# Kernel optimization log

Hardware: AMD Instinct MI355X
Metric: run time of the kernel (lower is better)

The kernel has to match this reference:

```python
import jax, jax.numpy as jnp
import numpy as np

N_PE = 100000   # num 'pe' nodes
N_R = 100000    # num 'router' nodes
E = 600000      # edges per relation
D_IN = 64       # input feature dim per node type
H = 128         # hidden_channels
G = 64          # graphs in batch


def setup_inputs() -> dict:
    key = jax.random.key(0)
    ks = jax.random.split(key, 20)
    inp = {}
    inp["x_pe"] = jax.random.normal(ks[0], (N_PE, D_IN), jnp.float32)
    inp["x_r"] = jax.random.normal(ks[1], (N_R, D_IN), jnp.float32)
    # edge_index per relation: row0 = src node ids, row1 = dst node ids
    inp["ei_per"] = jax.random.randint(ks[2], (2, E), 0, N_PE, jnp.int32)   # pe -> router
    inp["ei_rpe"] = jax.random.randint(ks[3], (2, E), 0, N_R, jnp.int32)    # router -> pe
    inp["ei_rr"] = jax.random.randint(ks[4], (2, E), 0, N_R, jnp.int32)     # router -> router
    inp["batch_pe"] = jnp.sort(jax.random.randint(ks[5], (N_PE,), 0, G, jnp.int32))
    inp["batch_r"] = jnp.sort(jax.random.randint(ks[6], (N_R,), 0, G, jnp.int32))
    # GraphConv params, relation axis ordered [pe->router, router->pe, router->router]
    s1 = 1.0 / np.sqrt(D_IN)
    s2 = 1.0 / np.sqrt(H)
    inp["Wrel1"] = jax.random.normal(ks[7], (3, D_IN, H), jnp.float32) * s1
    inp["brel1"] = jnp.zeros((3, H), jnp.float32)
    inp["Wroot1"] = jax.random.normal(ks[8], (3, D_IN, H), jnp.float32) * s1
    inp["Wrel23"] = jax.random.normal(ks[9], (2, 3, H, H), jnp.float32) * s2
    inp["brel23"] = jnp.zeros((2, 3, H), jnp.float32)
    inp["Wroot23"] = jax.random.normal(ks[10], (2, 3, H, H), jnp.float32) * s2
    # per-node-type MLP heads, type axis ordered [pe, router]
    inp["mlp_W1"] = jax.random.normal(ks[11], (2, H, 5), jnp.float32) * s2
    inp["mlp_b1"] = jnp.zeros((2, 5), jnp.float32)
    inp["mlp_W2"] = jax.random.normal(ks[12], (2, 5, 1), jnp.float32) * (1.0 / np.sqrt(5.0))
    inp["mlp_b2"] = jnp.zeros((2, 1), jnp.float32)
    inp["out_W"] = jax.random.normal(ks[13], (2, 1), jnp.float32) * (1.0 / np.sqrt(2.0))
    inp["out_b"] = jnp.zeros((1,), jnp.float32)
    return inp


def _hetero_graphconv(x_pe, x_r, ei_per, ei_rpe, ei_rr, Wrel, brel, Wroot):
    # GraphConv: lin_rel(scatter_add(x_src)) + lin_root(x_dst); to_hetero sums per dst type.
    agg_r_from_pe = jax.ops.segment_sum(x_pe[ei_per[0]], ei_per[1], num_segments=N_R)
    agg_pe_from_r = jax.ops.segment_sum(x_r[ei_rpe[0]], ei_rpe[1], num_segments=N_PE)
    agg_r_from_r = jax.ops.segment_sum(x_r[ei_rr[0]], ei_rr[1], num_segments=N_R)
    o_pe = agg_pe_from_r @ Wrel[1] + brel[1] + x_pe @ Wroot[1]
    o_r = (agg_r_from_pe @ Wrel[0] + brel[0] + x_r @ Wroot[0]) \
        + (agg_r_from_r @ Wrel[2] + brel[2] + x_r @ Wroot[2])
    return o_pe, o_r


def reference(x_pe, x_r, ei_per, ei_rpe, ei_rr, batch_pe, batch_r,
              Wrel1, brel1, Wroot1, Wrel23, brel23, Wroot23,
              mlp_W1, mlp_b1, mlp_W2, mlp_b2, out_W, out_b):
    h_pe, h_r = _hetero_graphconv(x_pe, x_r, ei_per, ei_rpe, ei_rr, Wrel1, brel1, Wroot1)
    h_pe, h_r = jax.nn.relu(h_pe), jax.nn.relu(h_r)
    h_pe, h_r = _hetero_graphconv(h_pe, h_r, ei_per, ei_rpe, ei_rr, Wrel23[0], brel23[0], Wroot23[0])
    h_pe, h_r = jax.nn.relu(h_pe), jax.nn.relu(h_r)
    h_pe, h_r = _hetero_graphconv(h_pe, h_r, ei_per, ei_rpe, ei_rr, Wrel23[1], brel23[1], Wroot23[1])
    gm_pe = jax.ops.segment_max(h_pe, batch_pe, num_segments=G)  # [G, H]
    gm_r = jax.ops.segment_max(h_r, batch_r, num_segments=G)
    def mlp(x, W1, b1, W2, b2):
        return jax.nn.relu(x @ W1 + b1) @ W2 + b2
    o_pe = mlp(gm_pe, mlp_W1[0], mlp_b1[0], mlp_W2[0], mlp_b2[0])  # [G, 1]
    o_r = mlp(gm_r, mlp_W1[1], mlp_b1[1], mlp_W2[1], mlp_b2[1])
    cat = jnp.concatenate([o_pe, o_r], axis=1)  # [G, 2]
    return cat @ out_W + out_b  # [G, 1]
```

## Files before the change

### kernel.cpp

```cpp
#include <hip/hip_runtime.h>
#include <cstddef>
#include <cstdint>

#define DIN 64
#define HID 128
#define NBKMAX 256
#define EPB 2048

typedef _Float16 half4v __attribute__((ext_vector_type(4)));
typedef _Float16 half8v __attribute__((ext_vector_type(8)));
typedef float f32x16 __attribute__((ext_vector_type(16)));

__device__ __forceinline__ unsigned encf(float f) {
    unsigned b = __float_as_uint(f);
    return (b & 0x80000000u) ? ~b : (b | 0x80000000u);
}
__device__ __forceinline__ float decf(unsigned u) {
    unsigned b = (u & 0x80000000u) ? (u & 0x7FFFFFFFu) : ~u;
    return __uint_as_float(b);
}

__global__ void matadd3_k(const float* a0, const float* b0f, float* o0, int n0,
                          const float* a1, const float* b1f, float* o1, int n1,
                          const float* a2, const float* b2f, float* o2, int n2) {
    int r = blockIdx.y;
    const float* a = r == 0 ? a0 : (r == 1 ? a1 : a2);
    const float* b = r == 0 ? b0f : (r == 1 ? b1f : b2f);
    float* o = r == 0 ? o0 : (r == 1 ? o1 : o2);
    int n = r == 0 ? n0 : (r == 1 ? n1 : n2);
    int i = blockIdx.x * 256 + threadIdx.x;
    if (i < n) o[i] = a[i] + b[i];
}

__global__ void conv_x2_k(const float* s0, _Float16* d0, int n40,
                          const float* s1, _Float16* d1, int n41) {
    int r = blockIdx.y;
    const float* s = r == 0 ? s0 : s1;
    _Float16* d = r == 0 ? d0 : d1;
    int n4 = r == 0 ? n40 : n41;
    int i = blockIdx.x * 256 + threadIdx.x;
    if (i >= n4) return;
    float4 v = *reinterpret_cast<const float4*>(&s[i * 4]);
    half4v h;
    h.x = (_Float16)v.x; h.y = (_Float16)v.y; h.z = (_Float16)v.z; h.w = (_Float16)v.w;
    *reinterpret_cast<half4v*>(&d[i * 4]) = h;
}

struct CW { const float* src; _Float16* dst; int K; int total; };
__global__ void conv_w7_k(CW c0, CW c1, CW c2, CW c3, CW c4, CW c5, CW c6) {
    CW J;
    switch (blockIdx.y) {
        case 0: J = c0; break; case 1: J = c1; break; case 2: J = c2; break;
        case 3: J = c3; break; case 4: J = c4; break; case 5: J = c5; break;
        default: J = c6; break;
    }
    int i = blockIdx.x * 256 + threadIdx.x;
    if (i >= J.total) return;
    int m = i / (J.K * HID);
    int rem = i % (J.K * HID);
    int k = rem / HID;
    int col = rem % HID;
    J.dst[(size_t)m * HID * J.K + (size_t)col * J.K + k] = (_Float16)J.src[i];
}

__global__ __launch_bounds__(256) void bhist_k(const int* e0, const int* e1, const int* e2, int E,
                                               int* c0, int* c1, int* c2) {
    int r = blockIdx.y;
    const int* ei = r == 0 ? e0 : (r == 1 ? e1 : e2);
    int* cnt = r == 0 ? c0 : (r == 1 ? c1 : c2);
    __shared__ int sc[NBKMAX];
    int t = threadIdx.x;
    sc[t] = 0;
    __syncthreads();
    int base = blockIdx.x * EPB;
    int n = min(EPB, E - base);
    for (int i = t; i < n; i += 256)
        atomicAdd(&sc[(unsigned)ei[E + base + i] >> 9], 1);
    __syncthreads();
    if (sc[t]) atomicAdd(&cnt[t], sc[t]);
}

__global__ __launch_bounds__(256) void bscan_k(int* c0, int* bb0, int* cu0, int* rp0, int n0,
                                               int* c1, int* bb1, int* cu1, int* rp1, int n1,
                                               int* c2, int* bb2, int* cu2, int* rp2, int n2,
                                               int E) {
    __shared__ int sh[256];
    int t = threadIdx.x;
    for (int r = 0; r < 3; ++r) {
        int* cnt = r == 0 ? c0 : (r == 1 ? c1 : c2);
        int* bb  = r == 0 ? bb0 : (r == 1 ? bb1 : bb2);
        int* cu  = r == 0 ? cu0 : (r == 1 ? cu1 : cu2);
        int* rp  = r == 0 ? rp0 : (r == 1 ? rp1 : rp2);
        int N    = r == 0 ? n0 : (r == 1 ? n1 : n2);
        int v = cnt[t];
        sh[t] = v;
        __syncthreads();
        for (int off = 1; off < 256; off <<= 1) {
            int val = (t >= off) ? sh[t - off] : 0;
            __syncthreads();
            sh[t] += val;
            __syncthreads();
        }
        int ex = sh[t] - v;
        bb[t] = ex;
        cu[t] = ex;
        if (t == 255) bb[256] = sh[255];
        if (t == 0) rp[N] = E;
        __syncthreads();
    }
}

__global__ __launch_bounds__(256) void bin_k(const int* e0, const int* e1, const int* e2, int E,
                                             int* cu0, int* cu1, int* cu2,
                                             unsigned* t0, unsigned* t1, unsigned* t2) {
    int r = blockIdx.y;
    const int* ei = r == 0 ? e0 : (r == 1 ? e1 : e2);
    int* gcur = r == 0 ? cu0 : (r == 1 ? cu1 : cu2);
    unsigned* temp = r == 0 ? t0 : (r == 1 ? t1 : t2);
    __shared__ unsigned pk[EPB];
    __shared__ unsigned short bkb[EPB];
    __shared__ int cnt[NBKMAX];
    __shared__ int scn[NBKMAX];
    __shared__ int rb[NBKMAX];
    int t = threadIdx.x;
    int base = blockIdx.x * EPB;
    int n = min(EPB, E - base);
    cnt[t] = 0;
    __syncthreads();
    for (int i = t; i < n; i += 256)
        atomicAdd(&cnt[(unsigned)ei[E + base + i] >> 9], 1);
    __syncthreads();
    {
        int v = cnt[t];
        scn[t] = v;
        __syncthreads();
        for (int off = 1; off < 256; off <<= 1) {
            int val = (t >= off) ? scn[t - off] : 0;
            __syncthreads();
            scn[t] += val;
            __syncthreads();
        }
        int ex = scn[t] - v;
        __syncthreads();
        scn[t] = ex;
    }
    {
        int c = cnt[t];
        rb[t] = c ? atomicAdd(&gcur[t], c) : 0;
        cnt[t] = 0;
    }
    __syncthreads();
    for (int i = t; i < n; i += 256) {
        int s = ei[base + i];
        int d = ei[E + base + i];
        int b = (unsigned)d >> 9;
        int slot = scn[b] + atomicAdd(&cnt[b], 1);
        pk[slot] = ((unsigned)s << 9) | (unsigned)(d & 511);
        bkb[slot] = (unsigned short)b;
    }
    __syncthreads();
    for (int i = t; i < n; i += 256) {
        int b = bkb[i];
        temp[rb[b] + (i - scn[b])] = pk[i];
    }
}

__global__ __launch_bounds__(256) void bcsr_k(const unsigned* t0, const unsigned* t1, const unsigned* t2,
                                              const int* bb0, const int* bb1, const int* bb2,
                                              int* rp0, int* rp1, int* rp2,
                                              int* a0, int* a1, int* a2,
                                              int n0, int n1, int n2) {
    int r = blockIdx.y;
    const unsigned* temp = r == 0 ? t0 : (r == 1 ? t1 : t2);
    const int* bb = r == 0 ? bb0 : (r == 1 ? bb1 : bb2);
    int* rp = r == 0 ? rp0 : (r == 1 ? rp1 : rp2);
    int* adj = r == 0 ? a0 : (r == 1 ? a1 : a2);
    int N = r == 0 ? n0 : (r == 1 ? n1 : n2);
    int b = blockIdx.x;
    int lo = bb[b], hi = bb[b + 1];
    __shared__ int cnt[512];
    __shared__ int sh[256];
    int t = threadIdx.x;
    cnt[t] = 0; cnt[t + 256] = 0;
    __syncthreads();
    for (int i = lo + t; i < hi; i += 256)
        atomicAdd(&cnt[temp[i] & 511], 1);
    __syncthreads();
    int c0 = cnt[2 * t], c1 = cnt[2 * t + 1];
    sh[t] = c0 + c1;
    __syncthreads();
    for (int off = 1; off < 256; off <<= 1) {
        int v = (t >= off) ? sh[t - off] : 0;
        __syncthreads();
        sh[t] += v;
        __syncthreads();
    }
    int pairExcl = sh[t] - (c0 + c1);
    __syncthreads();
    int e0x = lo + pairExcl;
    int e1x = e0x + c0;
    cnt[2 * t] = e0x;
    cnt[2 * t + 1] = e1x;
    int nodeBase = b * 512;
    if (nodeBase + 2 * t < N) rp[nodeBase + 2 * t] = e0x;
    if (nodeBase + 2 * t + 1 < N) rp[nodeBase + 2 * t + 1] = e1x;
    __syncthreads();
    for (int i = lo + t; i < hi; i += 256) {
        unsigned p = temp[i];
        int pos = atomicAdd(&cnt[p & 511], 1);
        adj[pos] = p >> 9;
    }
}

struct AJob { const _Float16* X; const int* rp; const int* adj; _Float16* AGG; int N; int gb; };
template <int D>
__global__ __launch_bounds__(256) void gather3_k(AJob a0, AJob a1, AJob a2) {
    int b = blockIdx.x;
    AJob J;
    if (b < a0.gb) { J = a0; }
    else if (b < a0.gb + a1.gb) { J = a1; b -= a0.gb; }
    else { J = a2; b -= a0.gb + a1.gb; }
    constexpr int TPN = D / 8;
    constexpr int NPB = 256 / TPN;
    int node = b * NPB + threadIdx.x / TPN;
    int lane = threadIdx.x % TPN;
    if (node >= J.N) return;
    int a = J.rp[node], e1 = J.rp[node + 1];
    float acc[8] = {0.f, 0.f, 0.f, 0.f, 0.f, 0.f, 0.f, 0.f};
    int e = a;
    for (; e + 4 <= e1; e += 4) {
        int s0 = J.adj[e], s1 = J.adj[e + 1], s2 = J.adj[e + 2], s3 = J.adj[e + 3];
        half8v v0 = *reinterpret_cast<const half8v*>(&J.X[(size_t)s0 * D + lane * 8]);
        half8v v1 = *reinterpret_cast<const half8v*>(&J.X[(size_t)s1 * D + lane * 8]);
        half8v v2 = *reinterpret_cast<const half8v*>(&J.X[(size_t)s2 * D + lane * 8]);
        half8v v3 = *reinterpret_cast<const half8v*>(&J.X[(size_t)s3 * D + lane * 8]);
#pragma unroll
        for (int i = 0; i < 8; ++i) acc[i] += (float)v0[i] + (float)v1[i] + (float)v2[i] + (float)v3[i];
    }
    for (; e < e1; ++e) {
        int s0 = J.adj[e];
        half8v v0 = *reinterpret_cast<const half8v*>(&J.X[(size_t)s0 * D + lane * 8]);
#pragma unroll
        for (int i = 0; i < 8; ++i) acc[i] += (float)v0[i];
    }
    half8v o;
#pragma unroll
    for (int i = 0; i < 8; ++i) o[i] = (_Float16)acc[i];
    *reinterpret_cast<half8v*>(&J.AGG[(size_t)node * D + lane * 8]) = o;
}

struct GJob {
    const _Float16* A0; const _Float16* A1; const _Float16* A2;
    const _Float16* W0; const _Float16* W1; const _Float16* W2;
    const float* b0; const float* b1;
    _Float16* O;
    int N; int total; int gb;
};

template <bool RELU>
__global__ __launch_bounds__(256) void gemm2_k(GJob j0, GJob j1, int K, int lg) {
    const bool second = ((int)blockIdx.x >= j0.gb);
    const GJob J = second ? j1 : j0;
    const int bx = blockIdx.x - (second ? j0.gb : 0);
    __shared__ _Float16 Alds[2][128 * 64];
    const int tid = threadIdx.x;
    const int lane = tid & 63;
    const int w = tid >> 6;
    const int wr = w & 1, wc = w >> 1;
    const int rowBase = bx * 128;

    f32x16 acc[2][2];
#pragma unroll
    for (int r = 0; r < 2; ++r)
#pragma unroll
        for (int c = 0; c < 2; ++c)
#pragma unroll
            for (int q = 0; q < 16; ++q) acc[r][c][q] = 0.0f;

    const _Float16* Ap[3] = {J.A0, J.A1, J.A2};

    const int row = tid & 127;
    const int kh = (tid >> 7) * 32;
    const int gr = rowBase + row;
    const bool rowOK = (gr < J.N);
    int offW[4];
#pragma unroll
    for (int j = 0; j < 4; ++j) {
        int t = (kh >> 4) + (j >> 1);
        int k8 = j & 1;
        offW[j] = (((row >> 5) * 4 + t) * 64 + (row & 31) + 32 * k8) * 8;
    }

    const int total = J.total;
    const int cmask = (1 << lg) - 1;

    auto ld = [&](int c, half8v h[4]) {
        int s = c >> lg;
        int k0 = (c & cmask) * 64;
        half8v z = {};
        h[0] = z; h[1] = z; h[2] = z; h[3] = z;
        if (rowOK) {
            const _Float16* p = Ap[s] + (size_t)gr * K + k0 + kh;
#pragma unroll
            for (int j = 0; j < 4; ++j) h[j] = *reinterpret_cast<const half8v*>(p + j * 8);
        }
    };

    half8v cur[4], nxt[4];
    ld(0, cur);
#pragma unroll
    for (int j = 0; j < 4; ++j) *reinterpret_cast<half8v*>(&Alds[0][offW[j]]) = cur[j];
    __syncthreads();

    for (int c = 0; c < total; ++c) {
        if (c + 1 < total) ld(c + 1, nxt);
        int s = c >> lg;
        int wk0 = (c & cmask) * 64;
        const _Float16* __restrict__ Wt = (s == 0) ? J.W0 : (s == 1 ? J.W1 : J.W2);
        const _Float16* buf = Alds[c & 1];
#pragma unroll
        for (int t = 0; t < 4; ++t) {
            half8v av[2], wv[2];
#pragma unroll
            for (int r = 0; r < 2; ++r) {
                int R = (wr * 2 + r) * 4 + t;
                av[r] = *reinterpret_cast<const half8v*>(&buf[(R * 64 + lane) * 8]);
            }
#pragma unroll
            for (int cc = 0; cc < 2; ++cc) {
                int col = wc * 64 + cc * 32 + (lane & 31);
                wv[cc] = *reinterpret_cast<const half8v*>(
                    &Wt[(size_t)col * K + wk0 + t * 16 + (lane >> 5) * 8]);
            }
#pragma unroll
            for (int r = 0; r < 2; ++r)
#pragma unroll
                for (int cc = 0; cc < 2; ++cc)
                    acc[r][cc] = __builtin_amdgcn_mfma_f32_32x32x16_f16(wv[cc], av[r], acc[r][cc], 0, 0, 0);
        }
        if (c + 1 < total) {
            _Float16* nb = Alds[(c + 1) & 1];
#pragma unroll
            for (int j = 0; j < 4; ++j) *reinterpret_cast<half8v*>(&nb[offW[j]]) = nxt[j];
        }
        __syncthreads();
    }

#pragma unroll
    for (int r = 0; r < 2; ++r) {
        int node = rowBase + (wr * 2 + r) * 32 + (lane & 31);
        if (node >= J.N) continue;
        _Float16* orow = J.O + (size_t)node * HID;
#pragma unroll
        for (int cc = 0; cc < 2; ++cc) {
            int fb_ = wc * 64 + cc * 32 + 4 * (lane >> 5);
#pragma unroll
            for (int g = 0; g < 4; ++g) {
                int f = fb_ + g * 8;
                float4 bv = *reinterpret_cast<const float4*>(&J.b0[f]);
                if (J.b1) {
                    float4 b2v = *reinterpret_cast<const float4*>(&J.b1[f]);
                    bv.x += b2v.x; bv.y += b2v.y; bv.z += b2v.z; bv.w += b2v.w;
                }
                half4v hv;
#pragma unroll
                for (int i = 0; i < 4; ++i) {
                    float v = acc[r][cc][g * 4 + i] + ((const float*)&bv)[i];
                    if (RELU) v = fmaxf(v, 0.f);
                    hv[i] = (_Float16)v;
                }
                *reinterpret_cast<half4v*>(&orow[f]) = hv;
            }
        }
    }
}

__global__ void seg_bounds2_k(const int* b0, int n0, int* s0,
                              const int* b1, int n1, int* s1, int G) {
    int r = blockIdx.x;
    const int* batch = r == 0 ? b0 : b1;
    int n = r == 0 ? n0 : n1;
    int* starts = r == 0 ? s0 : s1;
    int g = threadIdx.x;
    if (g > G) return;
    int lo = 0, hi = n;
    while (lo < hi) {
        int mid = (lo + hi) >> 1;
        if (batch[mid] < g) lo = mid + 1; else hi = mid;
    }
    starts[g] = lo;
}

__global__ __launch_bounds__(128) void seg_max2_k(const _Float16* H0, const int* st0, unsigned* g0,
                                                  const _Float16* H1, const int* st1, unsigned* g1) {
    int z = blockIdx.z;
    const _Float16* Hf = z == 0 ? H0 : H1;
    const int* starts = z == 0 ? st0 : st1;
    unsigned* gmU = z == 0 ? g0 : g1;
    int g = blockIdx.x;
    int sub = blockIdx.y;
    int SUB = gridDim.y;
    int f = threadIdx.x;
    int s0 = starts[g], s1 = starts[g + 1];
    int len = s1 - s0;
    if (len <= 0) return;
    int chunk = (len + SUB - 1) / SUB;
    int a = s0 + sub * chunk;
    int b = min(a + chunk, s1);
    if (a >= b) return;
    float m = -__builtin_huge_valf();
    for (int n = a; n < b; ++n) m = fmaxf(m, (float)Hf[(size_t)n * HID + f]);
    atomicMax(&gmU[g * HID + f], encf(m));
}

__global__ void head_k(const unsigned* __restrict__ gmU_pe, const unsigned* __restrict__ gmU_r,
                       const float* __restrict__ W1, const float* __restrict__ b1,
                       const float* __restrict__ W2, const float* __restrict__ b2,
                       const float* __restrict__ oW, const float* __restrict__ ob,
                       float* __restrict__ out, int G) {
    int g = threadIdx.x;
    if (g >= G) return;
    float vals[2];
#pragma unroll
    for (int t = 0; t < 2; ++t) {
        const unsigned* gm = t ? gmU_r : gmU_pe;
        float z[5];
#pragma unroll
        for (int j = 0; j < 5; ++j) z[j] = b1[t * 5 + j];
        for (int f = 0; f < HID; ++f) {
            float x = decf(gm[g * HID + f]);
#pragma unroll
            for (int j = 0; j < 5; ++j) z[j] = fmaf(x, W1[t * HID * 5 + f * 5 + j], z[j]);
        }
        float o = b2[t];
#pragma unroll
        for (int j = 0; j < 5; ++j) o = fmaf(fmaxf(z[j], 0.f), W2[t * 5 + j], o);
        vals[t] = o;
    }
    out[g] = vals[0] * oW[0] + vals[1] * oW[1] + ob[0];
}

extern "C" void kernel_launch(void* const* d_in, const int* in_sizes, int n_in,
                              void* d_out, int out_size, void* d_ws, size_t ws_size,
                              hipStream_t stream) {
    const float* x_pe    = (const float*)d_in[0];
    const float* x_r     = (const float*)d_in[1];
    const int* ei_per    = (const int*)d_in[2];
    const int* ei_rpe    = (const int*)d_in[3];
    const int* ei_rr     = (const int*)d_in[4];
    const int* batch_pe  = (const int*)d_in[5];
    const int* batch_r   = (const int*)d_in[6];
    const float* Wrel1   = (const float*)d_in[7];
    const float* brel1   = (const float*)d_in[8];
    const float* Wroot1  = (const float*)d_in[9];
    const float* Wrel23  = (const float*)d_in[10];
    const float* brel23  = (const float*)d_in[11];
    const float* Wroot23 = (const float*)d_in[12];
    const float* mlp_W1  = (const float*)d_in[13];
    const float* mlp_b1  = (const float*)d_in[14];
    const float* mlp_W2  = (const float*)d_in[15];
    const float* mlp_b2  = (const float*)d_in[16];
    const float* out_W   = (const float*)d_in[17];
    const float* out_b   = (const float*)d_in[18];
    float* out = (float*)d_out;

    const int N_PE = in_sizes[0] / DIN;
    const int N_R  = in_sizes[1] / DIN;
    const int E    = in_sizes[2] / 2;
    const int G    = out_size;
    const int NMAX = (N_PE > N_R) ? N_PE : N_R;
    const size_t SZM = (size_t)NMAX * HID;

    _Float16* H1 = (_Float16*)d_ws;
    _Float16* H2 = H1 + SZM;
    _Float16* H3 = H2 + SZM;
    _Float16* H4 = H3 + SZM;
    _Float16* H5 = H4 + SZM;
    _Float16* xh_pe = H5 + SZM;
    _Float16* xh_r  = xh_pe + (size_t)N_PE * DIN;
    float* wsum1 = (float*)(xh_r + (size_t)N_R * DIN);
    float* wsum2 = wsum1 + DIN * HID;
    float* wsum3 = wsum2 + HID * HID;
    _Float16* wt_rel1    = (_Float16*)(wsum3 + HID * HID);
    _Float16* wt_root1pe = wt_rel1 + 3 * DIN * HID;
    _Float16* wt_wsum1   = wt_root1pe + DIN * HID;
    _Float16* wt_rel23   = wt_wsum1 + DIN * HID;
    _Float16* wt_root23  = wt_rel23 + 6 * HID * HID;
    _Float16* wt_wsum2   = wt_root23 + 6 * HID * HID;
    _Float16* wt_wsum3   = wt_wsum2 + HID * HID;
    unsigned* gmU_pe = (unsigned*)(wt_wsum3 + HID * HID);
    unsigned* gmU_r  = gmU_pe + G * HID;
    int* starts_pe = (int*)(gmU_r + G * HID);
    int* starts_r  = starts_pe + (G + 1);
    int* bktCnt = starts_r + (G + 1);
    int* bb     = bktCnt + 3 * NBKMAX;
    int* gcur   = bb + 3 * (NBKMAX + 1);
    int* csr    = gcur + 3 * NBKMAX;
    const size_t relstride = (size_t)(NMAX + 1) + 2 * (size_t)E + 16;

    int* rp[3]; int* adjp[3]; unsigned* tmp[3];
    const int Nds[3] = {N_R, N_PE, N_R};
    for (int r = 0; r < 3; ++r) {
        int* rowptr = csr + (size_t)r * relstride;
        rp[r] = rowptr;
        adjp[r] = rowptr + (Nds[r] + 1);
        tmp[r] = (unsigned*)(adjp[r] + E);
    }

    const int gpe = (N_PE + 127) / 128, grr = (N_R + 127) / 128;

    {
        dim3 g((16384 + 255) / 256, 3);
        matadd3_k<<<g, 256, 0, stream>>>(
            Wroot1, Wroot1 + 2 * DIN * HID, wsum1, DIN * HID,
            Wroot23, Wroot23 + 2 * HID * HID, wsum2, HID * HID,
            Wroot23 + 3 * HID * HID, Wroot23 + 5 * HID * HID, wsum3, HID * HID);
    }
    {
        int n40 = N_PE * DIN / 4, n41 = N_R * DIN / 4;
        int nmax = n40 > n41 ? n40 : n41;
        dim3 g((nmax + 255) / 256, 2);
        conv_x2_k<<<g, 256, 0, stream>>>(x_pe, xh_pe, n40, x_r, xh_r, n41);
    }
    {
        CW c0{Wrel1, wt_rel1, DIN, 3 * DIN * HID};
        CW c1{Wroot1 + 1 * DIN * HID, wt_root1pe, DIN, DIN * HID};
        CW c2{wsum1, wt_wsum1, DIN, DIN * HID};
        CW c3{Wrel23, wt_rel23, HID, 6 * HID * HID};
        CW c4{Wroot23, wt_root23, HID, 6 * HID * HID};
        CW c5{wsum2, wt_wsum2, HID, HID * HID};
        CW c6{wsum3, wt_wsum3, HID, HID * HID};
        dim3 g((6 * HID * HID + 255) / 256, 7);
        conv_w7_k<<<g, 256, 0, stream>>>(c0, c1, c2, c3, c4, c5, c6);
    }
    {
        hipMemsetAsync(bktCnt, 0, 3 * NBKMAX * sizeof(int), stream);
        int eb = (E + EPB - 1) / EPB;
        dim3 gh(eb, 3);
        bhist_k<<<gh, 256, 0, stream>>>(ei_per, ei_rpe, ei_rr, E,
                                        bktCnt, bktCnt + NBKMAX, bktCnt + 2 * NBKMAX);
        bscan_k<<<1, 256, 0, stream>>>(
            bktCnt, bb, gcur, rp[0], Nds[0],
            bktCnt + NBKMAX, bb + (NBKMAX + 1), gcur + NBKMAX, rp[1], Nds[1],
            bktCnt + 2 * NBKMAX, bb + 2 * (NBKMAX + 1), gcur + 2 * NBKMAX, rp[2], Nds[2], E);
        bin_k<<<gh, 256, 0, stream>>>(ei_per, ei_rpe, ei_rr, E,
                                      gcur, gcur + NBKMAX, gcur + 2 * NBKMAX,
                                      tmp[0], tmp[1], tmp[2]);
        dim3 gc(NBKMAX, 3);
        bcsr_k<<<gc, 256, 0, stream>>>(tmp[0], tmp[1], tmp[2],
                                       bb, bb + (NBKMAX + 1), bb + 2 * (NBKMAX + 1),
                                       rp[0], rp[1], rp[2],
                                       adjp[0], adjp[1], adjp[2],
                                       Nds[0], Nds[1], Nds[2]);
    }

    {
        AJob a0{xh_r, rp[1], adjp[1], H1, N_PE, (N_PE + 31) / 32};
        AJob a1{xh_pe, rp[0], adjp[0], H2, N_R, (N_R + 31) / 32};
        AJob a2{xh_r, rp[2], adjp[2], H3, N_R, (N_R + 31) / 32};
        gather3_k<DIN><<<a0.gb + a1.gb + a2.gb, 256, 0, stream>>>(a0, a1, a2);
        GJob jp{H1, xh_pe, nullptr,
                wt_rel1 + 1 * DIN * HID, wt_root1pe, nullptr,
                brel1 + HID, nullptr, H4, N_PE, 2, gpe};
        GJob jr{H2, H3, xh_r,
                wt_rel1, wt_rel1 + 2 * DIN * HID, wt_wsum1,
                brel1, brel1 + 2 * HID, H5, N_R, 3, grr};
        gemm2_k<true><<<gpe + grr, 256, 0, stream>>>(jp, jr, DIN, 0);
    }
    {
        AJob a0{H5, rp[1], adjp[1], H1, N_PE, (N_PE + 15) / 16};
        AJob a1{H4, rp[0], adjp[0], H2, N_R, (N_R + 15) / 16};
        AJob a2{H5, rp[2], adjp[2], H3, N_R, (N_R + 15) / 16};
        gather3_k<HID><<<a0.gb + a1.gb + a2.gb, 256, 0, stream>>>(a0, a1, a2);
        GJob jp{H1, H4, nullptr,
                wt_rel23 + 1 * HID * HID, wt_root23 + 1 * HID * HID, nullptr,
                brel23 + HID, nullptr, H1, N_PE, 2 * 2, gpe};
        GJob jr{H2, H3, H5,
                wt_rel23, wt_rel23 + 2 * HID * HID, wt_wsum2,
                brel23, brel23 + 2 * HID, H2, N_R, 3 * 2, grr};
        gemm2_k<true><<<gpe + grr, 256, 0, stream>>>(jp, jr, HID, 1);
    }
    {
        AJob a0{H2, rp[1], adjp[1], H3, N_PE, (N_PE + 15) / 16};
        AJob a1{H1, rp[0], adjp[0], H4, N_R, (N_R + 15) / 16};
        AJob a2{H2, rp[2], adjp[2], H5, N_R, (N_R + 15) / 16};
        gather3_k<HID><<<a0.gb + a1.gb + a2.gb, 256, 0, stream>>>(a0, a1, a2);
        GJob jp{H3, H1, nullptr,
                wt_rel23 + 4 * HID * HID, wt_root23 + 4 * HID * HID, nullptr,
                brel23 + 4 * HID, nullptr, H3, N_PE, 2 * 2, gpe};
        GJob jr{H4, H5, H2,
                wt_rel23 + 3 * HID * HID, wt_rel23 + 5 * HID * HID, wt_wsum3,
                brel23 + 3 * HID, brel23 + 5 * HID, H4, N_R, 3 * 2, grr};
        gemm2_k<false><<<gpe + grr, 256, 0, stream>>>(jp, jr, HID, 1);
    }

    seg_bounds2_k<<<2, 128, 0, stream>>>(batch_pe, N_PE, starts_pe, batch_r, N_R, starts_r, G);
    hipMemsetAsync(gmU_pe, 0, 2 * (size_t)G * HID * sizeof(unsigned), stream);
    dim3 gs(G, 16, 2);
    seg_max2_k<<<gs, 128, 0, stream>>>(H3, starts_pe, gmU_pe, H4, starts_r, gmU_r);
    head_k<<<1, 64, 0, stream>>>(gmU_pe, gmU_r, mlp_W1, mlp_b1, mlp_W2, mlp_b2, out_W, out_b, out, G);
}
```

Baseline: 629.4 us.

## Stage weight tiles in LDS for GEMM and fuse root-weight sums into conversion

The GEMM kernel now loads each 128x64 weight chunk into shared memory alongside the A tile, instead of having every wave read weight fragments straight from global memory. The A tile goes from double-buffered to single-buffered, with an extra barrier per chunk. Separately, the matadd kernel that summed root weights is folded into the weight conversion kernel through an optional second source, removing one launch and only converting the root weights actually used. The extra barrier and lost double buffering may expose load latency.

```diff
diff --git a/kernel.cpp b/kernel.cpp
--- a/kernel.cpp
+++ b/kernel.cpp
@@ -18,18 +18,6 @@
 __device__ __forceinline__ float decf(unsigned u) {
     unsigned b = (u & 0x80000000u) ? (u & 0x7FFFFFFFu) : ~u;
     return __uint_as_float(b);
-}
-
-__global__ void matadd3_k(const float* a0, const float* b0f, float* o0, int n0,
-                          const float* a1, const float* b1f, float* o1, int n1,
-                          const float* a2, const float* b2f, float* o2, int n2) {
-    int r = blockIdx.y;
-    const float* a = r == 0 ? a0 : (r == 1 ? a1 : a2);
-    const float* b = r == 0 ? b0f : (r == 1 ? b1f : b2f);
-    float* o = r == 0 ? o0 : (r == 1 ? o1 : o2);
-    int n = r == 0 ? n0 : (r == 1 ? n1 : n2);
-    int i = blockIdx.x * 256 + threadIdx.x;
-    if (i < n) o[i] = a[i] + b[i];
 }
 
 __global__ void conv_x2_k(const float* s0, _Float16* d0, int n40,
@@ -46,13 +34,13 @@
     *reinterpret_cast<half4v*>(&d[i * 4]) = h;
 }
 
-struct CW { const float* src; _Float16* dst; int K; int total; };
-__global__ void conv_w7_k(CW c0, CW c1, CW c2, CW c3, CW c4, CW c5, CW c6) {
+struct CW { const float* src; const float* src2; _Float16* dst; int K; int total; };
+__global__ void conv_w8_k(CW c0, CW c1, CW c2, CW c3, CW c4, CW c5, CW c6, CW c7) {
     CW J;
     switch (blockIdx.y) {
         case 0: J = c0; break; case 1: J = c1; break; case 2: J = c2; break;
         case 3: J = c3; break; case 4: J = c4; break; case 5: J = c5; break;
-        default: J = c6; break;
+        case 6: J = c6; break; default: J = c7; break;
     }
     int i = blockIdx.x * 256 + threadIdx.x;
     if (i >= J.total) return;
@@ -60,7 +48,9 @@
     int rem = i % (J.K * HID);
     int k = rem / HID;
     int col = rem % HID;
-    J.dst[(size_t)m * HID * J.K + (size_t)col * J.K + k] = (_Float16)J.src[i];
+    float v = J.src[i];
+    if (J.src2) v += J.src2[i];
+    J.dst[(size_t)m * HID * J.K + (size_t)col * J.K + k] = (_Float16)v;
 }
 
 __global__ __launch_bounds__(256) void bhist_k(const int* e0, const int* e1, const int* e2, int E,
@@ -262,7 +252,8 @@
     const bool second = ((int)blockIdx.x >= j0.gb);
     const GJob J = second ? j1 : j0;
     const int bx = blockIdx.x - (second ? j0.gb : 0);
-    __shared__ _Float16 Alds[2][128 * 64];
+    __shared__ _Float16 Alds[128 * 64];
+    __shared__ _Float16 Wlds[128 * 64];
     const int tid = threadIdx.x;
     const int lane = tid & 63;
     const int w = tid >> 6;
@@ -283,18 +274,18 @@
     const int kh = (tid >> 7) * 32;
     const int gr = rowBase + row;
     const bool rowOK = (gr < J.N);
-    int offW[4];
+    int offS[4];
 #pragma unroll
     for (int j = 0; j < 4; ++j) {
         int t = (kh >> 4) + (j >> 1);
         int k8 = j & 1;
-        offW[j] = (((row >> 5) * 4 + t) * 64 + (row & 31) + 32 * k8) * 8;
+        offS[j] = (((row >> 5) * 4 + t) * 64 + (row & 31) + 32 * k8) * 8;
     }
 
     const int total = J.total;
     const int cmask = (1 << lg) - 1;
 
-    auto ld = [&](int c, half8v h[4]) {
+    auto ldA = [&](int c, half8v h[4]) {
         int s = c >> lg;
         int k0 = (c & cmask) * 64;
         half8v z = {};
@@ -305,45 +296,51 @@
             for (int j = 0; j < 4; ++j) h[j] = *reinterpret_cast<const half8v*>(p + j * 8);
         }
     };
-
-    half8v cur[4], nxt[4];
-    ld(0, cur);
-#pragma unroll
-    for (int j = 0; j < 4; ++j) *reinterpret_cast<half8v*>(&Alds[0][offW[j]]) = cur[j];
+    auto ldW = [&](int c, half8v h[4]) {
+        int s = c >> lg;
+        int k0 = (c & cmask) * 64;
+        const _Float16* __restrict__ Wt = (s == 0) ? J.W0 : (s == 1 ? J.W1 : J.W2);
+        const _Float16* p = Wt + (size_t)row * K + k0 + kh;
+#pragma unroll
+        for (int j = 0; j < 4; ++j) h[j] = *reinterpret_cast<const half8v*>(p + j * 8);
+    };
+
+    half8v ra[4], rw[4];
+    ldA(0, ra); ldW(0, rw);
+#pragma unroll
+    for (int j = 0; j < 4; ++j) {
+        *reinterpret_cast<half8v*>(&Alds[offS[j]]) = ra[j];
+        *reinterpret_cast<half8v*>(&Wlds[offS[j]]) = rw[j];
+    }
     __syncthreads();
 
     for (int c = 0; c < total; ++c) {
-        if (c + 1 < total) ld(c + 1, nxt);
-        int s = c >> lg;
-        int wk0 = (c & cmask) * 64;
-        const _Float16* __restrict__ Wt = (s == 0) ? J.W0 : (s == 1 ? J.W1 : J.W2);
-        const _Float16* buf = Alds[c & 1];
+        const bool more = (c + 1 < total);
+        if (more) { ldA(c + 1, ra); ldW(c + 1, rw); }
 #pragma unroll
         for (int t = 0; t < 4; ++t) {
             half8v av[2], wv[2];
 #pragma unroll
-            for (int r = 0; r < 2; ++r) {
-                int R = (wr * 2 + r) * 4 + t;
-                av[r] = *reinterpret_cast<const half8v*>(&buf[(R * 64 + lane) * 8]);
-            }
-#pragma unroll
-            for (int cc = 0; cc < 2; ++cc) {
-                int col = wc * 64 + cc * 32 + (lane & 31);
-                wv[cc] = *reinterpret_cast<const half8v*>(
-                    &Wt[(size_t)col * K + wk0 + t * 16 + (lane >> 5) * 8]);
-            }
+            for (int r = 0; r < 2; ++r)
+                av[r] = *reinterpret_cast<const half8v*>(&Alds[(((wr * 2 + r) * 4 + t) * 64 + lane) * 8]);
+#pragma unroll
+            for (int cc = 0; cc < 2; ++cc)
+                wv[cc] = *reinterpret_cast<const half8v*>(&Wlds[(((wc * 2 + cc) * 4 + t) * 64 + lane) * 8]);
 #pragma unroll
             for (int r = 0; r < 2; ++r)
 #pragma unroll
                 for (int cc = 0; cc < 2; ++cc)
                     acc[r][cc] = __builtin_amdgcn_mfma_f32_32x32x16_f16(wv[cc], av[r], acc[r][cc], 0, 0, 0);
         }
-        if (c + 1 < total) {
-            _Float16* nb = Alds[(c + 1) & 1];
-#pragma unroll
-            for (int j = 0; j < 4; ++j) *reinterpret_cast<half8v*>(&nb[offW[j]]) = nxt[j];
-        }
-        __syncthreads();
+        __syncthreads();
+        if (more) {
+#pragma unroll
+            for (int j = 0; j < 4; ++j) {
+                *reinterpret_cast<half8v*>(&Alds[offS[j]]) = ra[j];
+                *reinterpret_cast<half8v*>(&Wlds[offS[j]]) = rw[j];
+            }
+            __syncthreads();
+        }
     }
 
 #pragma unroll
@@ -478,15 +475,13 @@
     _Float16* H5 = H4 + SZM;
     _Float16* xh_pe = H5 + SZM;
     _Float16* xh_r  = xh_pe + (size_t)N_PE * DIN;
-    float* wsum1 = (float*)(xh_r + (size_t)N_R * DIN);
-    float* wsum2 = wsum1 + DIN * HID;
-    float* wsum3 = wsum2 + HID * HID;
-    _Float16* wt_rel1    = (_Float16*)(wsum3 + HID * HID);
+    _Float16* wt_rel1    = xh_r + (size_t)N_R * DIN;
     _Float16* wt_root1pe = wt_rel1 + 3 * DIN * HID;
     _Float16* wt_wsum1   = wt_root1pe + DIN * HID;
     _Float16* wt_rel23   = wt_wsum1 + DIN * HID;
-    _Float16* wt_root23  = wt_rel23 + 6 * HID * HID;
-    _Float16* wt_wsum2   = wt_root23 + 6 * HID * HID;
+    _Float16* wt_root_l2 = wt_rel23 + 6 * HID * HID;
+    _Float16* wt_root_l3 = wt_root_l2 + HID * HID;
+    _Float16* wt_wsum2   = wt_root_l3 + HID * HID;
     _Float16* wt_wsum3   = wt_wsum2 + HID * HID;
     unsigned* gmU_pe = (unsigned*)(wt_wsum3 + HID * HID);
     unsigned* gmU_r  = gmU_pe + G * HID;
@@ -510,28 +505,22 @@
     const int gpe = (N_PE + 127) / 128, grr = (N_R + 127) / 128;
 
     {
-        dim3 g((16384 + 255) / 256, 3);
-        matadd3_k<<<g, 256, 0, stream>>>(
-            Wroot1, Wroot1 + 2 * DIN * HID, wsum1, DIN * HID,
-            Wroot23, Wroot23 + 2 * HID * HID, wsum2, HID * HID,
-            Wroot23 + 3 * HID * HID, Wroot23 + 5 * HID * HID, wsum3, HID * HID);
-    }
-    {
         int n40 = N_PE * DIN / 4, n41 = N_R * DIN / 4;
         int nmax = n40 > n41 ? n40 : n41;
         dim3 g((nmax + 255) / 256, 2);
         conv_x2_k<<<g, 256, 0, stream>>>(x_pe, xh_pe, n40, x_r, xh_r, n41);
     }
     {
-        CW c0{Wrel1, wt_rel1, DIN, 3 * DIN * HID};
-        CW c1{Wroot1 + 1 * DIN * HID, wt_root1pe, DIN, DIN * HID};
-        CW c2{wsum1, wt_wsum1, DIN, DIN * HID};
-        CW c3{Wrel23, wt_rel23, HID, 6 * HID * HID};
-        CW c4{Wroot23, wt_root23, HID, 6 * HID * HID};
-        CW c5{wsum2, wt_wsum2, HID, HID * HID};
-        CW c6{wsum3, wt_wsum3, HID, HID * HID};
-        dim3 g((6 * HID * HID + 255) / 256, 7);
-        conv_w7_k<<<g, 256, 0, stream>>>(c0, c1, c2, c3, c4, c5, c6);
+        CW c0{Wrel1, nullptr, wt_rel1, DIN, 3 * DIN * HID};
+        CW c1{Wroot1 + 1 * DIN * HID, nullptr, wt_root1pe, DIN, DIN * HID};
+        CW c2{Wroot1, Wroot1 + 2 * DIN * HID, wt_wsum1, DIN, DIN * HID};
+        CW c3{Wrel23, nullptr, wt_rel23, HID, 6 * HID * HID};
+        CW c4{Wroot23 + 1 * HID * HID, nullptr, wt_root_l2, HID, HID * HID};
+        CW c5{Wroot23 + 4 * HID * HID, nullptr, wt_root_l3, HID, HID * HID};
+        CW c6{Wroot23, Wroot23 + 2 * HID * HID, wt_wsum2, HID, HID * HID};
+        CW c7{Wroot23 + 3 * HID * HID, Wroot23 + 5 * HID * HID, wt_wsum3, HID, HID * HID};
+        dim3 g((6 * HID * HID + 255) / 256, 8);
+        conv_w8_k<<<g, 256, 0, stream>>>(c0, c1, c2, c3, c4, c5, c6, c7);
     }
     {
         hipMemsetAsync(bktCnt, 0, 3 * NBKMAX * sizeof(int), stream);
@@ -573,7 +562,7 @@
         AJob a2{H5, rp[2], adjp[2], H3, N_R, (N_R + 15) / 16};
         gather3_k<HID><<<a0.gb + a1.gb + a2.gb, 256, 0, stream>>>(a0, a1, a2);
         GJob jp{H1, H4, nullptr,
-                wt_rel23 + 1 * HID * HID, wt_root23 + 1 * HID * HID, nullptr,
+                wt_rel23 + 1 * HID * HID, wt_root_l2, nullptr,
                 brel23 + HID, nullptr, H1, N_PE, 2 * 2, gpe};
         GJob jr{H2, H3, H5,
                 wt_rel23, wt_rel23 + 2 * HID * HID, wt_wsum2,
@@ -586,7 +575,7 @@
         AJob a2{H2, rp[2], adjp[2], H5, N_R, (N_R + 15) / 16};
         gather3_k<HID><<<a0.gb + a1.gb + a2.gb, 256, 0, stream>>>(a0, a1, a2);
         GJob jp{H3, H1, nullptr,
-                wt_rel23 + 4 * HID * HID, wt_root23 + 4 * HID * HID, nullptr,
+                wt_rel23 + 4 * HID * HID, wt_root_l3, nullptr,
                 brel23 + 4 * HID, nullptr, H3, N_PE, 2 * 2, gpe};
         GJob jr{H4, H5, H2,
                 wt_rel23 + 3 * HID * HID, wt_rel23 + 5 * HID * HID, wt_wsum3,
```

After: 622.7 us. No clear change (-1.1%).
